# Kernel tuning notes

Measured on AMD Instinct MI355X. Metric: run time of the kernel, lower is better.

## Reference

```python
import jax, jax.numpy as jnp
import numpy as np


def setup_inputs() -> dict:
    key = jax.random.key(0)
    ks = jax.random.split(key, 32)
    def rn(i, shape, s=0.02):
        return jax.random.normal(ks[i], shape, dtype=jnp.float32) * s
    z = lambda n: jnp.zeros((n,), dtype=jnp.float32)
    return {
        'c2': rn(0, (8, 256, 112, 112), 1.0),
        'c3': rn(1, (8, 512, 56, 56), 1.0),
        'c4': rn(2, (8, 1024, 28, 28), 1.0),
        'c5': rn(3, (8, 2048, 14, 14), 1.0),
        'lat_w0': rn(4, (256, 256)),  'lat_b0': z(256),
        'lat_w1': rn(5, (512, 256)),  'lat_b1': z(256),
        'lat_w2': rn(6, (1024, 256)), 'lat_b2': z(256),
        'lat_w3': rn(7, (2048, 256)), 'lat_b3': z(256),
        'sp_w1': rn(8, (2048, 512)), 'sp_b1': z(512),
        'sp_w2': rn(9, (512, 4)),    'sp_b2': z(4),
        'qkv_w': rn(10, (256, 768)), 'qkv_b': z(768),
        'proj_w': rn(11, (256, 256)), 'proj_b': z(256),
        'gat_W': rn(12, (4, 256, 256)),
        'gat_a': rn(13, (4, 512)),
        'out_w': rn(14, (1024, 256)), 'out_b': z(256),
        'label_emb': rn(15, (80, 256), 1.0),
        'spec_w1': rn(16, (256, 128)), 'spec_b1': z(128),
        'spec_w2': rn(17, (128, 80)),  'spec_b2': z(80),
        'spat_w1': rn(18, (256, 128)), 'spat_b1': z(128),
        'spat_w2': rn(19, (128, 80)),  'spat_b2': z(80),
        'gate_w': rn(20, (256, 80)), 'gate_b': z(80),
        'unc_w': rn(21, (256, 80)),  'unc_b': z(80),
    }


def _forward(c2, c3, c4, c5,
             lat_w0, lat_b0, lat_w1, lat_b1, lat_w2, lat_b2, lat_w3, lat_b3,
             sp_w1, sp_b1, sp_w2, sp_b2,
             qkv_w, qkv_b, proj_w, proj_b,
             gat_W, gat_a, out_w, out_b, label_emb,
             spec_w1, spec_b1, spec_w2, spec_b2,
             spat_w1, spat_b1, spat_w2, spat_b2,
             gate_w, gate_b, unc_w, unc_b):
    B = c2.shape[0]
    L = label_emb.shape[0]
    C = 256
    # --- DynamicScaleAwareFPN ---
    pooled = c5.mean(axis=(2, 3))                                   # [B,2048]
    sw = jax.nn.softmax(jax.nn.relu(pooled @ sp_w1 + sp_b1) @ sp_w2 + sp_b2, axis=1)  # [B,4]
    H, W = c2.shape[2], c2.shape[3]
    feats = (c2, c3, c4, c5)
    lws = (lat_w0, lat_w1, lat_w2, lat_w3)
    lbs = (lat_b0, lat_b1, lat_b2, lat_b3)
    fused = jnp.zeros((B, C, H, W), dtype=c2.dtype)
    for i in range(4):  # fixed 4 scales
        l = jnp.einsum('bchw,cd->bdhw', feats[i], lws[i]) + lbs[i][None, :, None, None]
        if l.shape[2] != H or l.shape[3] != W:
            l = jax.image.resize(l, (B, C, H, W), method='bilinear')  # align_corners=False
        fused = fused + l * sw[:, i, None, None, None]
    # --- DeformableAttention (N=H*W > max_tokens=196 -> adaptive pool to 14x14) ---
    th = 14
    x = fused.reshape(B, C, th, H // th, th, W // th).mean(axis=(3, 5))  # exact adaptive avg pool
    x = x.reshape(B, C, th * th).transpose(0, 2, 1)                      # [B,196,C]
    N, nh, hd = th * th, 8, C // 8
    qkv = (x @ qkv_w + qkv_b).reshape(B, N, 3, nh, hd).transpose(2, 0, 3, 1, 4)
    q, k, v = qkv[0], qkv[1], qkv[2]                                     # [B,nh,N,hd]
    attn = jax.nn.softmax(jnp.einsum('bhnd,bhmd->bhnm', q, k) * (hd ** -0.5), axis=-1)
    xo = jnp.einsum('bhnm,bhmd->bhnd', attn, v).transpose(0, 2, 1, 3).reshape(B, N, C)
    xo = xo @ proj_w + proj_b
    gctx = xo.mean(axis=1)                                               # [B,C]
    # --- CrossLabelSemanticGraph (4 GAT heads) ---
    lf = label_emb[None] + gctx[:, None, :]                              # [B,L,C]
    def gat(Wm, avec):
        Wx = lf @ Wm                                                     # [B,L,C]
        # a([Wx_i ; Wx_j]) = Wx_i @ a1 + Wx_j @ a2  (avoids O(L^2*2C) tensor)
        s1 = Wx @ avec[:C]                                               # [B,L]
        s2 = Wx @ avec[C:]                                               # [B,L]
        e = jax.nn.leaky_relu(s1[:, :, None] + s2[:, None, :], 0.2)      # [B,L,L]
        att = jax.nn.softmax(e, axis=2)
        return att @ Wx, att
    heads, atts = jax.vmap(gat)(gat_W, gat_a)                            # [4,B,L,C],[4,B,L,L]
    concat = jnp.moveaxis(heads, 0, 2).reshape(B, L, 4 * C)              # head-order concat
    graph = concat @ out_w + out_b                                       # [B,L,C]
    agg = graph.mean(axis=1)                                             # [B,C]
    # --- SpectralSpatialFusion (dropout inactive at eval) ---
    spec = jax.nn.relu(agg @ spec_w1 + spec_b1) @ spec_w2 + spec_b2
    spat = jax.nn.relu(agg @ spat_w1 + spat_b1) @ spat_w2 + spat_b2
    gate = jax.nn.sigmoid(agg @ gate_w + gate_b)
    logits = gate * spec + (1.0 - gate) * spat
    # --- UncertaintyHead ---
    alpha = jax.nn.softplus(agg @ unc_w + unc_b) + 1.0
    unc = L / jnp.sum(alpha, axis=1, keepdims=True)
    return (logits, spec, spat, gate, unc, sw, atts)


def reference(c2, c3, c4, c5,
              lat_w0, lat_b0, lat_w1, lat_b1, lat_w2, lat_b2, lat_w3, lat_b3,
              sp_w1, sp_b1, sp_w2, sp_b2,
              qkv_w, qkv_b, proj_w, proj_b,
              gat_W, gat_a, out_w, out_b, label_emb,
              spec_w1, spec_b1, spec_w2, spec_b2,
              spat_w1, spat_b1, spat_w2, spat_b2,
              gate_w, gate_b, unc_w, unc_b):
    return _forward(c2, c3, c4, c5,
                    lat_w0, lat_b0, lat_w1, lat_b1, lat_w2, lat_b2, lat_w3, lat_b3,
                    sp_w1, sp_b1, sp_w2, sp_b2,
                    qkv_w, qkv_b, proj_w, proj_b,
                    gat_W, gat_a, out_w, out_b, label_emb,
                    spec_w1, spec_b1, spec_w2, spec_b2,
                    spat_w1, spat_b1, spat_w2, spat_b2,
                    gate_w, gate_b, unc_w, unc_b)
```

## Files before the change

### kernel.cpp

```cpp
#include <hip/hip_runtime.h>
#include <math.h>

typedef __attribute__((ext_vector_type(8))) short bshort8;
typedef __attribute__((ext_vector_type(4))) float f32x4;

#define DI __device__ __forceinline__

DI unsigned short f2bf(float x) {
    unsigned int u = __builtin_bit_cast(unsigned int, x);
    u += 0x7fffu + ((u >> 16) & 1u);
    return (unsigned short)(u >> 16);
}

DI bshort8 pack8(const float* v) {
    bshort8 r;
    #pragma unroll
    for (int j = 0; j < 8; j++) r[j] = (short)f2bf(v[j]);
    return r;
}

DI f32x4 mfma16(bshort8 a, bshort8 b, f32x4 c) {
    return __builtin_amdgcn_mfma_f32_16x16x32_bf16(a, b, c, 0, 0, 0);
}

__device__ const float W14[14][3] = {
    {0.875f, 0.125f, 0.f},
    {0.125f, 0.75f, 0.125f}, {0.125f, 0.75f, 0.125f}, {0.125f, 0.75f, 0.125f},
    {0.125f, 0.75f, 0.125f}, {0.125f, 0.75f, 0.125f}, {0.125f, 0.75f, 0.125f},
    {0.125f, 0.75f, 0.125f}, {0.125f, 0.75f, 0.125f}, {0.125f, 0.75f, 0.125f},
    {0.125f, 0.75f, 0.125f}, {0.125f, 0.75f, 0.125f}, {0.125f, 0.75f, 0.125f},
    {0.125f, 0.875f, 0.f}};
__device__ const float W28[14][4] = {
    {0.5f, 0.4375f, 0.0625f, 0.f},
    {0.0625f, 0.4375f, 0.4375f, 0.0625f}, {0.0625f, 0.4375f, 0.4375f, 0.0625f},
    {0.0625f, 0.4375f, 0.4375f, 0.0625f}, {0.0625f, 0.4375f, 0.4375f, 0.0625f},
    {0.0625f, 0.4375f, 0.4375f, 0.0625f}, {0.0625f, 0.4375f, 0.4375f, 0.0625f},
    {0.0625f, 0.4375f, 0.4375f, 0.0625f}, {0.0625f, 0.4375f, 0.4375f, 0.0625f},
    {0.0625f, 0.4375f, 0.4375f, 0.0625f}, {0.0625f, 0.4375f, 0.4375f, 0.0625f},
    {0.0625f, 0.4375f, 0.4375f, 0.0625f}, {0.0625f, 0.4375f, 0.4375f, 0.0625f},
    {0.0625f, 0.4375f, 0.5f, 0.f}};
__device__ const float W56[14][6] = {
    {0.25f, 0.25f, 0.25f, 0.21875f, 0.03125f, 0.f},
    {0.03125f, 0.21875f, 0.25f, 0.25f, 0.21875f, 0.03125f},
    {0.03125f, 0.21875f, 0.25f, 0.25f, 0.21875f, 0.03125f},
    {0.03125f, 0.21875f, 0.25f, 0.25f, 0.21875f, 0.03125f},
    {0.03125f, 0.21875f, 0.25f, 0.25f, 0.21875f, 0.03125f},
    {0.03125f, 0.21875f, 0.25f, 0.25f, 0.21875f, 0.03125f},
    {0.03125f, 0.21875f, 0.25f, 0.25f, 0.21875f, 0.03125f},
    {0.03125f, 0.21875f, 0.25f, 0.25f, 0.21875f, 0.03125f},
    {0.03125f, 0.21875f, 0.25f, 0.25f, 0.21875f, 0.03125f},
    {0.03125f, 0.21875f, 0.25f, 0.25f, 0.21875f, 0.03125f},
    {0.03125f, 0.21875f, 0.25f, 0.25f, 0.21875f, 0.03125f},
    {0.03125f, 0.21875f, 0.25f, 0.25f, 0.21875f, 0.03125f},
    {0.03125f, 0.21875f, 0.25f, 0.25f, 0.21875f, 0.03125f},
    {0.03125f, 0.21875f, 0.25f, 0.25f, 0.25f, 0.f}};

DI void pool_body112(const float* __restrict__ src, unsigned short* __restrict__ dst,
                     unsigned blk, unsigned t)
{
    unsigned id = blk * 256u + t;
    unsigned p = id / 196u;
    unsigned r = id - p * 196u;
    unsigned ti = r / 14u, tj = r - ti * 14u;
    unsigned b = p >> 8, cin = p & 255u;
    const float* plane = src + (size_t)p * 12544;
    const float4* p4 = (const float4*)(plane + (size_t)(ti * 8) * 112 + tj * 8);
    float4 rv[16];
    #pragma unroll
    for (int i = 0; i < 8; i++) { rv[2 * i] = p4[i * 28]; rv[2 * i + 1] = p4[i * 28 + 1]; }
    float acc = 0.f;
    #pragma unroll
    for (int i = 0; i < 16; i++) acc += (rv[i].x + rv[i].y) + (rv[i].z + rv[i].w);
    dst[(size_t)cin * 1568 + b * 196 + r] = f2bf(acc * (1.f / 64.f));
}

__global__ __launch_bounds__(256) void pool_all(
    const float* __restrict__ c2, const float* __restrict__ c3,
    const float* __restrict__ c4, const float* __restrict__ c5,
    unsigned short* __restrict__ pf0, unsigned short* __restrict__ pf1,
    unsigned short* __restrict__ pf2, unsigned short* __restrict__ pf3,
    float* __restrict__ pooled)
{
    __shared__ alignas(16) float ls[3136];
    unsigned bx = blockIdx.x, t = threadIdx.x;

    if (bx < 1568u) {
        pool_body112(c2, pf0, bx, t);
        return;
    }
    if (bx < 5664u) {
        unsigned p = bx - 1568u;
        unsigned b = p >> 9, cin = p & 511u;
        const float* plane = c3 + (size_t)p * 3136;
        float4* l4 = (float4*)ls;
        const float4* s4 = (const float4*)plane;
        for (int i = t; i < 784; i += 256) l4[i] = s4[i];
        __syncthreads();
        if (t < 196) {
            int ti = t / 14, tj = t - ti * 14;
            int hs = 4 * ti - 1; if (hs < 0) hs = 0;
            int ws = 4 * tj - 1; if (ws < 0) ws = 0;
            float acc = 0.f;
            #pragma unroll
            for (int i = 0; i < 6; i++) {
                int hi = hs + i; if (hi > 55) hi = 55;
                const float* row = ls + hi * 56;
                float rs = 0.f;
                #pragma unroll
                for (int j = 0; j < 6; j++) {
                    int wj = ws + j; if (wj > 55) wj = 55;
                    rs += W56[tj][j] * row[wj];
                }
                acc += W56[ti][i] * rs;
            }
            pf1[(size_t)cin * 1568 + b * 196 + t] = f2bf(acc);
        }
        return;
    }
    if (bx < 13856u) {
        unsigned p = bx - 5664u;
        unsigned b = p >> 10, cin = p & 1023u;
        const float* plane = c4 + (size_t)p * 784;
        float4* l4 = (float4*)ls;
        const float4* s4 = (const float4*)plane;
        if (t < 196) l4[t] = s4[t];
        __syncthreads();
        if (t < 196) {
            int ti = t / 14, tj = t - ti * 14;
            int hs = 2 * ti - 1; if (hs < 0) hs = 0;
            int ws = 2 * tj - 1; if (ws < 0) ws = 0;
            float acc = 0.f;
            #pragma unroll
            for (int i = 0; i < 4; i++) {
                int hi = hs + i; if (hi > 27) hi = 27;
                const float* row = ls + hi * 28;
                float rs = 0.f;
                #pragma unroll
                for (int j = 0; j < 4; j++) {
                    int wj = ws + j; if (wj > 27) wj = 27;
                    rs += W28[tj][j] * row[wj];
                }
                acc += W28[ti][i] * rs;
            }
            pf2[(size_t)cin * 1568 + b * 196 + t] = f2bf(acc);
        }
        return;
    }
    {
        unsigned g = bx - 13856u;
        int wid = t >> 6, lane = t & 63;
        unsigned p = g * 4 + wid;
        unsigned b = p >> 11, cin = p & 2047u;
        const float* plane = c5 + (size_t)p * 196;
        float a0 = plane[lane];
        float a1 = plane[64 + lane];
        float a2 = plane[128 + lane];
        float a3 = (lane < 4) ? plane[192 + lane] : 0.f;
        float* lw = ls + wid * 200;
        lw[lane] = a0; lw[64 + lane] = a1; lw[128 + lane] = a2;
        if (lane < 4) lw[192 + lane] = a3;
        float v = a0 + a1 + a2 + a3;
        #pragma unroll
        for (int off = 32; off > 0; off >>= 1) v += __shfl_xor(v, off, 64);
        if (lane == 0) pooled[p] = v * (1.f / 196.f);
        __syncthreads();
        unsigned short* dst = pf3 + (size_t)cin * 1568 + b * 196;
        #pragma unroll
        for (int rr = 0; rr < 4; rr++) {
            int r = rr * 64 + lane;
            if (r < 196) {
                int ti = r / 14, tj = r - ti * 14;
                int hs = ti - 1; if (hs < 0) hs = 0;
                int ws = tj - 1; if (ws < 0) ws = 0;
                float acc = 0.f;
                #pragma unroll
                for (int i = 0; i < 3; i++) {
                    int hi = hs + i; if (hi > 13) hi = 13;
                    const float* row = lw + hi * 14;
                    float rs = 0.f;
                    #pragma unroll
                    for (int j = 0; j < 3; j++) {
                        int wj = ws + j; if (wj > 13) wj = 13;
                        rs += W14[tj][j] * row[wj];
                    }
                    acc += W14[ti][i] * rs;
                }
                dst[r] = f2bf(acc);
            }
        }
    }
}

__global__ __launch_bounds__(512) void sw_part(
    const float* __restrict__ pooled, const float* __restrict__ sp_w1,
    float* __restrict__ partial,
    const float* __restrict__ gat_W, const float* __restrict__ gat_a,
    float* __restrict__ Wa)
{
    int t = threadIdx.x;
    if (blockIdx.y >= 8) {
        int e = (blockIdx.y - 8) * 8 + blockIdx.x;
        int h = e >> 2, q = e & 3;
        __shared__ float a1[256], a2[256];
        if (t < 256) { a1[t] = gat_a[h * 512 + t]; a2[t] = gat_a[h * 512 + 256 + t]; }
        __syncthreads();
        int w = t >> 6, lane = t & 63;
        #pragma unroll
        for (int ci = 0; ci < 8; ci++) {
            int c = q * 64 + w * 8 + ci;
            const float* row = gat_W + (size_t)h * 65536 + (size_t)c * 256;
            float p1 = 0.f, p2 = 0.f;
            #pragma unroll
            for (int jj = 0; jj < 4; jj++) {
                float v = row[lane + 64 * jj];
                p1 += v * a1[lane + 64 * jj];
                p2 += v * a2[lane + 64 * jj];
            }
            #pragma unroll
            for (int off = 32; off > 0; off >>= 1) {
                p1 += __shfl_xor(p1, off, 64);
                p2 += __shfl_xor(p2, off, 64);
            }
            if (lane == 0) { Wa[h * 512 + c] = p1; Wa[h * 512 + 256 + c] = p2; }
        }
        return;
    }
    int b = blockIdx.x, kc = blockIdx.y;
    __shared__ float ps[256];
    if (t < 256) ps[t] = pooled[b * 2048 + kc * 256 + t];
    __syncthreads();
    float acc = 0.f;
    const float* w = sp_w1 + (size_t)(kc * 256) * 512 + t;
    #pragma unroll 8
    for (int c = 0; c < 256; c++) acc += ps[c] * w[(size_t)c * 512];
    partial[((size_t)b * 8 + kc) * 512 + t] = acc;
}

__global__ __launch_bounds__(512) void sw_fin(
    const float* __restrict__ partial, const float* __restrict__ sp_b1,
    const float* __restrict__ sp_w2, const float* __restrict__ sp_b2,
    const float* __restrict__ lb0, const float* __restrict__ lb1,
    const float* __restrict__ lb2, const float* __restrict__ lb3,
    const float* __restrict__ lemb, const float* __restrict__ Wa,
    float* __restrict__ sw_out, float* __restrict__ xtok,
    float* __restrict__ ldot)
{
    int b = blockIdx.x, t = threadIdx.x;
    __shared__ float h[512];
    __shared__ float s4s[4];
    __shared__ float swl[4];
    __shared__ float bf_s[256];
    float a = sp_b1[t];
    #pragma unroll
    for (int kc = 0; kc < 8; kc++) a += partial[((size_t)b * 8 + kc) * 512 + t];
    h[t] = fmaxf(a, 0.f);
    __syncthreads();
    int wv = t >> 6, lane = t & 63;
    if (wv < 4) {
        float acc = 0.f;
        #pragma unroll
        for (int i = 0; i < 8; i++) {
            int idx = lane + 64 * i;
            acc += h[idx] * sp_w2[idx * 4 + wv];
        }
        #pragma unroll
        for (int off = 32; off > 0; off >>= 1) acc += __shfl_xor(acc, off, 64);
        if (lane == 0) s4s[wv] = acc + sp_b2[wv];
    }
    __syncthreads();
    if (t == 0) {
        float mx = fmaxf(fmaxf(s4s[0], s4s[1]), fmaxf(s4s[2], s4s[3]));
        float e0 = expf(s4s[0] - mx), e1 = expf(s4s[1] - mx);
        float e2 = expf(s4s[2] - mx), e3 = expf(s4s[3] - mx);
        float inv = 1.f / (e0 + e1 + e2 + e3);
        swl[0] = e0 * inv; swl[1] = e1 * inv; swl[2] = e2 * inv; swl[3] = e3 * inv;
        for (int o = 0; o < 4; o++) sw_out[b * 4 + o] = swl[o];
    }
    __syncthreads();
    if (t < 256)
        bf_s[t] = swl[0] * lb0[t] + swl[1] * lb1[t] + swl[2] * lb2[t] + swl[3] * lb3[t];
    {
        int pair = t >> 6;
        #pragma unroll
        for (int r = 0; r < 10; r++) {
            int l = b * 10 + r;
            const float* le = lemb + l * 256 + lane * 4;
            const float* wa = Wa + pair * 256 + lane * 4;
            float p = le[0] * wa[0] + le[1] * wa[1] + le[2] * wa[2] + le[3] * wa[3];
            #pragma unroll
            for (int off = 32; off > 0; off >>= 1) p += __shfl_xor(p, off, 64);
            if (lane == 0) ldot[l * 8 + pair] = p;
        }
    }
    __syncthreads();
    int c = t & 255, half = t >> 8;
    float bv = bf_s[c];
    float* xb = xtok + (size_t)b * 196 * 256 + c;
    for (int r = half; r < 196; r += 2) xb[(size_t)r * 256] = bv;
}

__global__ __launch_bounds__(256) void lateral_slice(
    const unsigned short* __restrict__ pf0, const unsigned short* __restrict__ pf1,
    const unsigned short* __restrict__ pf2, const unsigned short* __restrict__ pf3,
    const float* __restrict__ w0, const float* __restrict__ w1,
    const float* __restrict__ w2, const float* __restrict__ w3,
    const float* __restrict__ sw, float* __restrict__ xtok)
{
    const int sArr[8]    = {0, 1, 2, 2, 3, 3, 3, 3};
    const int koffArr[8] = {0, 0, 0, 512, 0, 512, 1024, 1536};
    const int klenArr[8] = {256, 512, 512, 512, 512, 512, 512, 512};
    int sl = blockIdx.y;
    int s = sArr[sl], koff = koffArr[sl], klen = klenArr[sl];
    const unsigned short* pf = (s == 0) ? pf0 : (s == 1) ? pf1 : (s == 2) ? pf2 : pf3;
    const float* W  = (s == 0) ? w0  : (s == 1) ? w1  : (s == 2) ? w2  : w3;

    int mt = blockIdx.x % 49, nt = blockIdx.x / 49;
    int m0 = mt * 32, n0 = nt * 64;
    __shared__ alignas(16) unsigned short As[1024];
    __shared__ alignas(16) unsigned short Bs[2048];
    int t = threadIdx.x, lane = t & 63, wid = t >> 6;
    int wm = wid >> 1, wn = wid & 1;
    f32x4 acc0 = {0, 0, 0, 0}, acc1 = {0, 0, 0, 0};

    int f = t & 63;
    int mA = m0 + ((t >> 6) & 1) * 16 + (f & 15);
    int kbA = (f >> 4) * 8;
    int nB = n0 + (t >> 6) * 16 + (f & 15);
    int kbB = (f >> 4) * 8;

    unsigned short ark[8];
    float br[8];
    auto loadA = [&](int k0) {
        if (t < 128) {
            const unsigned short* base = pf + (size_t)(koff + k0 + kbA) * 1568 + mA;
            #pragma unroll
            for (int j = 0; j < 8; j++) ark[j] = base[(size_t)j * 1568];
        }
    };
    auto loadB = [&](int k0) {
        const float* base = W + (size_t)(koff + k0 + kbB) * 256 + nB;
        #pragma unroll
        for (int j = 0; j < 8; j++) br[j] = base[(size_t)j * 256];
    };

    loadA(0); loadB(0);
    for (int k0 = 0; k0 < klen; k0 += 32) {
        if (t < 128) {
            bshort8 v8;
            #pragma unroll
            for (int j = 0; j < 8; j++) v8[j] = (short)ark[j];
            *(bshort8*)&As[(((t >> 6) & 1) * 512 + f * 8)] = v8;
        }
        *(bshort8*)&Bs[((t >> 6) * 512 + f * 8)] = pack8(br);
        __syncthreads();
        if (k0 + 32 < klen) { loadA(k0 + 32); loadB(k0 + 32); }
        bshort8 av = *(const bshort8*)&As[wm * 512 + lane * 8];
        bshort8 bv0 = *(const bshort8*)&Bs[(wn * 2 + 0) * 512 + lane * 8];
        bshort8 bv1 = *(const bshort8*)&Bs[(wn * 2 + 1) * 512 + lane * 8];
        acc0 = mfma16(av, bv0, acc0);
        acc1 = mfma16(av, bv1, acc1);
        __syncthreads();
    }
    int col0 = n0 + wn * 32 + (lane & 15);
    int rbase = m0 + wm * 16 + ((lane >> 4) << 2);
    #pragma unroll
    for (int r = 0; r < 4; r++) {
        int m = rbase + r;
        float swv = sw[(m / 196) * 4 + s];
        atomicAdd(&xtok[(size_t)m * 256 + col0], acc0[r] * swv);
        atomicAdd(&xtok[(size_t)m * 256 + col0 + 16], acc1[r] * swv);
    }
}

template <bool B_IS_KXN>
__global__ __launch_bounds__(256) void gemm_kernel(
    const float* __restrict__ Ab, int lda, long long sAy, long long sAz,
    const float* __restrict__ Bb, int ldb, long long sBy, long long sBz,
    float* __restrict__ Cb, int ldc, long long sCy, long long sCz,
    const float* __restrict__ bias, int M, int N, int K,
    float alpha, int mtiles)
{
    const float* A = Ab + blockIdx.y * sAy + blockIdx.z * sAz;
    const float* B = Bb + blockIdx.y * sBy + blockIdx.z * sBz;
    float* C = Cb + blockIdx.y * sCy + blockIdx.z * sCz;
    int mt = blockIdx.x % mtiles, nt = blockIdx.x / mtiles;
    int m0 = mt * 32, n0 = nt * 64;
    __shared__ alignas(16) unsigned short As[1024];
    __shared__ alignas(16) unsigned short Bs[2048];
    int t = threadIdx.x, lane = t & 63, wid = t >> 6;
    int wm = wid >> 1, wn = wid & 1;
    f32x4 acc0 = {0, 0, 0, 0}, acc1 = {0, 0, 0, 0};

    int f = t & 63;
    int mA = m0 + ((t >> 6) & 1) * 16 + (f & 15);
    int kbA = (f >> 4) * 8;
    int nB = n0 + (t >> 6) * 16 + (f & 15);
    int kbB = (f >> 4) * 8;

    float ar[8], br[8];
    auto loadA = [&](int k0) {
        if (t < 128) {
            int kb = k0 + kbA;
            if (mA < M && kb + 8 <= K) {
                const float4* p = (const float4*)(A + (size_t)mA * lda + kb);
                float4 u = p[0], v = p[1];
                ar[0] = u.x; ar[1] = u.y; ar[2] = u.z; ar[3] = u.w;
                ar[4] = v.x; ar[5] = v.y; ar[6] = v.z; ar[7] = v.w;
            } else {
                #pragma unroll
                for (int j = 0; j < 8; j++) {
                    int k = kb + j;
                    ar[j] = (mA < M && k < K) ? A[(size_t)mA * lda + k] : 0.f;
                }
            }
        }
    };
    auto loadB = [&](int k0) {
        int kb = k0 + kbB;
        if constexpr (B_IS_KXN) {
            #pragma unroll
            for (int j = 0; j < 8; j++) {
                int k = kb + j;
                br[j] = (k < K && nB < N) ? B[(size_t)k * ldb + nB] : 0.f;
            }
        } else {
            if (nB < N && kb + 8 <= K) {
                const float4* p = (const float4*)(B + (size_t)nB * ldb + kb);
                float4 u = p[0], v = p[1];
                br[0] = u.x; br[1] = u.y; br[2] = u.z; br[3] = u.w;
                br[4] = v.x; br[5] = v.y; br[6] = v.z; br[7] = v.w;
            } else {
                #pragma unroll
                for (int j = 0; j < 8; j++) {
                    int k = kb + j;
                    br[j] = (nB < N && k < K) ? B[(size_t)nB * ldb + k] : 0.f;
                }
            }
        }
    };

    loadA(0); loadB(0);
    for (int k0 = 0; k0 < K; k0 += 32) {
        if (t < 128) *(bshort8*)&As[(((t >> 6) & 1) * 512 + f * 8)] = pack8(ar);
        *(bshort8*)&Bs[((t >> 6) * 512 + f * 8)] = pack8(br);
        __syncthreads();
        if (k0 + 32 < K) { loadA(k0 + 32); loadB(k0 + 32); }
        bshort8 av = *(const bshort8*)&As[wm * 512 + lane * 8];
        bshort8 bv0 = *(const bshort8*)&Bs[(wn * 2 + 0) * 512 + lane * 8];
        bshort8 bv1 = *(const bshort8*)&Bs[(wn * 2 + 1) * 512 + lane * 8];
        acc0 = mfma16(av, bv0, acc0);
        acc1 = mfma16(av, bv1, acc1);
        __syncthreads();
    }
    int col0 = n0 + wn * 32 + (lane & 15);
    int rbase = m0 + wm * 16 + ((lane >> 4) << 2);
    #pragma unroll
    for (int r = 0; r < 4; r++) {
        int m = rbase + r;
        if (m < M) {
            if (col0 < N) {
                float v = acc0[r] * alpha;
                if (bias) v += bias[col0];
                C[(size_t)m * ldc + col0] = v;
            }
            int c1 = col0 + 16;
            if (c1 < N) {
                float v = acc1[r] * alpha;
                if (bias) v += bias[c1];
                C[(size_t)m * ldc + c1] = v;
            }
        }
    }
}

__global__ __launch_bounds__(256) void fused_attn(
    const float* __restrict__ qkv, float* __restrict__ xo)
{
    int mt = blockIdx.x, h = blockIdx.y, b = blockIdx.z;
    const float* Qb = qkv + (size_t)b * 150528 + h * 32;
    const float* Kb = Qb + 256;
    const float* Vb = Qb + 512;

    __shared__ alignas(16) unsigned short As[1024];
    __shared__ alignas(16) unsigned short Bs[2048];
    __shared__ float Ss[32 * 256];

    int t = threadIdx.x, lane = t & 63, wid = t >> 6;
    int wm = wid >> 1, wn = wid & 1;
    int f = t & 63;
    int m0 = mt * 32;

    if (t < 128) {
        float ar[8];
        int mA = m0 + ((t >> 6) & 1) * 16 + (f & 15);
        int kb = (f >> 4) * 8;
        if (mA < 196) {
            const float4* p = (const float4*)(Qb + (size_t)mA * 768 + kb);
            float4 u = p[0], v = p[1];
            ar[0] = u.x; ar[1] = u.y; ar[2] = u.z; ar[3] = u.w;
            ar[4] = v.x; ar[5] = v.y; ar[6] = v.z; ar[7] = v.w;
        } else {
            #pragma unroll
            for (int j = 0; j < 8; j++) ar[j] = 0.f;
        }
        *(bshort8*)&As[(((t >> 6) & 1) * 512 + f * 8)] = pack8(ar);
    }

    {
        int nBl = (t >> 6) * 16 + (f & 15);
        int kbB = (f >> 4) * 8;
        float br[8];
        auto loadB = [&](int g) {
            int key = g * 64 + nBl;
            if (key < 196) {
                const float4* p = (const float4*)(Kb + (size_t)key * 768 + kbB);
                float4 u = p[0], v = p[1];
                br[0] = u.x; br[1] = u.y; br[2] = u.z; br[3] = u.w;
                br[4] = v.x; br[5] = v.y; br[6] = v.z; br[7] = v.w;
            } else {
                #pragma unroll
                for (int j = 0; j < 8; j++) br[j] = 0.f;
            }
        };
        loadB(0);
        for (int g = 0; g < 4; g++) {
            __syncthreads();
            *(bshort8*)&Bs[((t >> 6) * 512 + f * 8)] = pack8(br);
            __syncthreads();
            if (g < 3) loadB(g + 1);
            f32x4 acc0 = {0, 0, 0, 0}, acc1 = {0, 0, 0, 0};
            bshort8 av = *(const bshort8*)&As[wm * 512 + lane * 8];
            bshort8 bv0 = *(const bshort8*)&Bs[(wn * 2 + 0) * 512 + lane * 8];
            bshort8 bv1 = *(const bshort8*)&Bs[(wn * 2 + 1) * 512 + lane * 8];
            acc0 = mfma16(av, bv0, acc0);
            acc1 = mfma16(av, bv1, acc1);
            int col0 = g * 64 + wn * 32 + (lane & 15);
            int rbase = wm * 16 + ((lane >> 4) << 2);
            #pragma unroll
            for (int r = 0; r < 4; r++) {
                Ss[(rbase + r) * 256 + col0]      = acc0[r] * 0.17677669529663687f;
                Ss[(rbase + r) * 256 + col0 + 16] = acc1[r] * 0.17677669529663687f;
            }
        }
    }
    __syncthreads();

    {
        #pragma unroll
        for (int i = 0; i < 8; i++) {
            float* p = Ss + (wid * 8 + i) * 256;
            float v0 = p[lane], v1 = p[64 + lane], v2 = p[128 + lane];
            float v3 = (lane < 4) ? p[192 + lane] : -1e30f;
            float mx = fmaxf(fmaxf(v0, v1), fmaxf(v2, v3));
            #pragma unroll
            for (int off = 32; off > 0; off >>= 1) mx = fmaxf(mx, __shfl_xor(mx, off, 64));
            float e0 = expf(v0 - mx), e1 = expf(v1 - mx), e2 = expf(v2 - mx);
            float e3 = (lane < 4) ? expf(v3 - mx) : 0.f;
            float sum = e0 + e1 + e2 + e3;
            #pragma unroll
            for (int off = 32; off > 0; off >>= 1) sum += __shfl_xor(sum, off, 64);
            float inv = 1.f / sum;
            p[lane] = e0 * inv;
            p[64 + lane] = e1 * inv;
            p[128 + lane] = e2 * inv;
            if (lane < 4) p[192 + lane] = e3 * inv;
            else          p[192 + lane] = 0.f;
        }
    }
    __syncthreads();

    {
        f32x4 acc0 = {0, 0, 0, 0}, acc1 = {0, 0, 0, 0};
        int nBl = (t >> 6) * 16 + (f & 15);
        int kbB = (f >> 4) * 8;
        int mAl = ((t >> 6) & 1) * 16 + (f & 15);
        int kbA = (f >> 4) * 8;
        float ar[8], br[8];
        auto loadA = [&](int k0) {
            if (t < 128) {
                #pragma unroll
                for (int j = 0; j < 8; j++) ar[j] = Ss[mAl * 256 + k0 + kbA + j];
            }
        };
        auto loadB = [&](int k0) {
            #pragma unroll
            for (int j = 0; j < 8; j++) {
                int k = k0 + kbB + j;
                br[j] = (k < 196 && nBl < 32) ? Vb[(size_t)k * 768 + nBl] : 0.f;
            }
        };
        loadA(0); loadB(0);
        for (int k0 = 0; k0 < 256; k0 += 32) {
            __syncthreads();
            if (t < 128) *(bshort8*)&As[(((t >> 6) & 1) * 512 + f * 8)] = pack8(ar);
            *(bshort8*)&Bs[((t >> 6) * 512 + f * 8)] = pack8(br);
            __syncthreads();
            if (k0 + 32 < 256) { loadA(k0 + 32); loadB(k0 + 32); }
            bshort8 av = *(const bshort8*)&As[wm * 512 + lane * 8];
            bshort8 bv0 = *(const bshort8*)&Bs[(wn * 2 + 0) * 512 + lane * 8];
            bshort8 bv1 = *(const bshort8*)&Bs[(wn * 2 + 1) * 512 + lane * 8];
            acc0 = mfma16(av, bv0, acc0);
            acc1 = mfma16(av, bv1, acc1);
        }
        int col0 = wn * 32 + (lane & 15);
        int rbase = wm * 16 + ((lane >> 4) << 2);
        if (col0 < 32) {
            #pragma unroll
            for (int r = 0; r < 4; r++) {
                int m = m0 + rbase + r;
                if (m < 196) {
                    xo[((size_t)b * 196 + m) * 256 + h * 32 + col0]      = acc0[r];
                    xo[((size_t)b * 196 + m) * 256 + h * 32 + col0 + 16] = acc1[r];
                }
            }
        }
    }
}

__global__ __launch_bounds__(1024) void tail1(
    const float* __restrict__ xo, const float* __restrict__ proj_w,
    const float* __restrict__ proj_b,
    const float* __restrict__ gat_W, const float* __restrict__ lemb,
    const float* __restrict__ Wa, const float* __restrict__ ldot,
    float* __restrict__ atts, float* __restrict__ hm_g)
{
    int b = blockIdx.x >> 2, h = blockIdx.x & 3;
    int t = threadIdx.x, lane = t & 63, wv = t >> 6;
    __shared__ float red[1024];
    __shared__ float xm[256];
    __shared__ float gctx_s[256];
    __shared__ float gdot_s[2];
    __shared__ float s12h[160];
    __shared__ float am_s[80];
    __shared__ float av_s[256];

    {
        int c = t & 255, sl = t >> 8;
        const float* base = xo + ((size_t)b * 196 + sl * 49) * 256 + c;
        float s = 0.f;
        #pragma unroll 7
        for (int i = 0; i < 49; i++) s += base[(size_t)i * 256];
        red[t] = s;
    }
    if (t < 80) am_s[t] = 0.f;
    __syncthreads();
    if (t < 256) xm[t] = (red[t] + red[256 + t] + red[512 + t] + red[768 + t]) * (1.f / 196.f);
    __syncthreads();

    {
        int n = t & 255, ks = t >> 8;
        float acc = 0.f;
        const float* w = proj_w + (size_t)(ks * 64) * 256 + n;
        #pragma unroll 8
        for (int i = 0; i < 64; i++) acc += xm[ks * 64 + i] * w[(size_t)i * 256];
        red[t] = acc;
    }
    __syncthreads();
    if (t < 256) gctx_s[t] = proj_b[t] + red[t] + red[256 + t] + red[512 + t] + red[768 + t];
    __syncthreads();

    if (wv < 2) {
        int pair = h * 2 + wv;
        const float* wa = Wa + pair * 256 + lane * 4;
        float p = gctx_s[lane * 4] * wa[0] + gctx_s[lane * 4 + 1] * wa[1]
                + gctx_s[lane * 4 + 2] * wa[2] + gctx_s[lane * 4 + 3] * wa[3];
        #pragma unroll
        for (int off = 32; off > 0; off >>= 1) p += __shfl_xor(p, off, 64);
        if (lane == 0) gdot_s[wv] = p;
    }
    __syncthreads();
    if (t < 160) {
        int q = t / 80, l = t - q * 80;
        s12h[t] = ldot[l * 8 + h * 2 + q] + gdot_s[q];
    }
    __syncthreads();

    {
        #pragma unroll
        for (int rr = 0; rr < 5; rr++) {
            int i = rr * 16 + wv;
            float s1i = s12h[i];
            const float* s2 = s12h + 80;
            float v0 = s1i + s2[lane]; v0 = v0 > 0.f ? v0 : 0.2f * v0;
            float v1 = -1e30f;
            if (lane < 16) { v1 = s1i + s2[64 + lane]; v1 = v1 > 0.f ? v1 : 0.2f * v1; }
            float mx = fmaxf(v0, v1);
            #pragma unroll
            for (int off = 32; off > 0; off >>= 1) mx = fmaxf(mx, __shfl_xor(mx, off, 64));
            float e0 = expf(v0 - mx), e1 = (lane < 16) ? expf(v1 - mx) : 0.f;
            float sum = e0 + e1;
            #pragma unroll
            for (int off = 32; off > 0; off >>= 1) sum += __shfl_xor(sum, off, 64);
            float inv = 1.f / sum;
            float* orow = atts + (size_t)h * 51200 + b * 6400 + i * 80;
            float p0 = e0 * inv;
            orow[lane] = p0;
            atomicAdd(&am_s[lane], p0);
            if (lane < 16) {
                float p1 = e1 * inv;
                orow[64 + lane] = p1;
                atomicAdd(&am_s[64 + lane], p1);
            }
        }
    }
    __syncthreads();

    {
        int n = t & 255, ks = t >> 8;
        float acc = 0.f;
        const float* le = lemb + n;
        #pragma unroll 5
        for (int l = ks * 20; l < ks * 20 + 20; l++) acc += am_s[l] * le[(size_t)l * 256];
        red[t] = acc;
    }
    __syncthreads();
    if (t < 256)
        av_s[t] = (red[t] + red[256 + t] + red[512 + t] + red[768 + t]) * (1.f / 80.f)
                + gctx_s[t];
    __syncthreads();
    {
        int n = t & 255, ks = t >> 8;
        float acc = 0.f;
        const float* w = gat_W + (size_t)h * 65536 + (size_t)(ks * 64) * 256 + n;
        #pragma unroll 8
        for (int i = 0; i < 64; i++) acc += av_s[ks * 64 + i] * w[(size_t)i * 256];
        red[t] = acc;
    }
    __syncthreads();
    if (t < 256)
        hm_g[(b * 4 + h) * 256 + t] = red[t] + red[256 + t] + red[512 + t] + red[768 + t];
}

__global__ __launch_bounds__(1024) void tail2(
    const float* __restrict__ hm_g,
    const float* __restrict__ out_w, const float* __restrict__ out_b,
    const float* __restrict__ spec_w1, const float* __restrict__ spec_b1,
    const float* __restrict__ spec_w2, const float* __restrict__ spec_b2,
    const float* __restrict__ spat_w1, const float* __restrict__ spat_b1,
    const float* __restrict__ spat_w2, const float* __restrict__ spat_b2,
    const float* __restrict__ gate_w, const float* __restrict__ gate_b,
    const float* __restrict__ unc_w, const float* __restrict__ unc_b,
    float* __restrict__ out)
{
    int b = blockIdx.x, t = threadIdx.x;
    __shared__ float red[1024];
    __shared__ float as_s[256];
    __shared__ float hb_s[256];
    __shared__ float fv_s[320];

    {
        int n = t & 255, ks = t >> 8;
        float acc = 0.f;
        const float* hv = hm_g + b * 1024 + ks * 256;
        const float* w = out_w + (size_t)(ks * 256) * 256 + n;
        #pragma unroll 8
        for (int k = 0; k < 256; k++) acc += hv[k] * w[(size_t)k * 256];
        red[t] = acc;
    }
    __syncthreads();
    if (t < 256) as_s[t] = out_b[t] + red[t] + red[256 + t] + red[512 + t] + red[768 + t];
    __syncthreads();

    {
        int u = t & 255, ks = t >> 8;
        int which = u >> 7, oo = u & 127;
        const float* w1 = which ? spat_w1 : spec_w1;
        float acc = 0.f;
        #pragma unroll 8
        for (int i = 0; i < 64; i++) {
            int k = ks * 64 + i;
            acc += as_s[k] * w1[(size_t)k * 128 + oo];
        }
        red[t] = acc;
    }
    __syncthreads();
    if (t < 256) {
        int which = t >> 7, oo = t & 127;
        const float* b1 = which ? spat_b1 : spec_b1;
        hb_s[t] = fmaxf(red[t] + red[256 + t] + red[512 + t] + red[768 + t] + b1[oo], 0.f);
    }
    __syncthreads();

    if (t < 960) {
        int sub = t / 320, u = t - sub * 320;
        int head = u / 80, o = u - head * 80;
        const float* wp; const float* src; int K;
        if (head == 0)      { wp = spec_w2; src = hb_s;       K = 128; }
        else if (head == 1) { wp = spat_w2; src = hb_s + 128; K = 128; }
        else if (head == 2) { wp = gate_w;  src = as_s;       K = 256; }
        else                { wp = unc_w;   src = as_s;       K = 256; }
        int k0 = (K * sub) / 3, k1 = (K * (sub + 1)) / 3;
        float acc = 0.f;
        for (int k = k0; k < k1; k++) acc += src[k] * wp[(size_t)k * 80 + o];
        red[sub * 320 + u] = acc;
    }
    __syncthreads();
    if (t < 320) {
        int head = t / 80, o = t - head * 80;
        const float* bp = head == 0 ? spec_b2 : head == 1 ? spat_b2 : head == 2 ? gate_b : unc_b;
        fv_s[t] = red[t] + red[320 + t] + red[640 + t] + bp[o];
    }
    __syncthreads();

    if (t < 80) {
        float sp = fv_s[t], st2 = fv_s[80 + t], gz = fv_s[160 + t], uz = fv_s[240 + t];
        float g = 1.f / (1.f + expf(-gz));
        out[b * 80 + t] = g * sp + (1.f - g) * st2;
        out[640 + b * 80 + t] = sp;
        out[1280 + b * 80 + t] = st2;
        out[1920 + b * 80 + t] = g;
        red[t] = log1pf(expf(uz)) + 1.f;
    }
    __syncthreads();
    if (t == 0) {
        float s = 0.f;
        for (int l = 0; l < 80; l++) s += red[l];
        out[2560 + b] = 80.f / s;
    }
}

extern "C" void kernel_launch(void* const* d_in, const int* in_sizes, int n_in,
                              void* d_out, int out_size, void* d_ws, size_t ws_size,
                              hipStream_t stream)
{
    (void)in_sizes; (void)n_in; (void)out_size; (void)ws_size;
    const float* c2 = (const float*)d_in[0];
    const float* c3 = (const float*)d_in[1];
    const float* c4 = (const float*)d_in[2];
    const float* c5 = (const float*)d_in[3];
    const float* lat_w0 = (const float*)d_in[4];
    const float* lat_b0 = (const float*)d_in[5];
    const float* lat_w1 = (const float*)d_in[6];
    const float* lat_b1 = (const float*)d_in[7];
    const float* lat_w2 = (const float*)d_in[8];
    const float* lat_b2 = (const float*)d_in[9];
    const float* lat_w3 = (const float*)d_in[10];
    const float* lat_b3 = (const float*)d_in[11];
    const float* sp_w1 = (const float*)d_in[12];
    const float* sp_b1 = (const float*)d_in[13];
    const float* sp_w2 = (const float*)d_in[14];
    const float* sp_b2 = (const float*)d_in[15];
    const float* qkv_w = (const float*)d_in[16];
    const float* qkv_b = (const float*)d_in[17];
    const float* proj_w = (const float*)d_in[18];
    const float* proj_b = (const float*)d_in[19];
    const float* gat_W = (const float*)d_in[20];
    const float* gat_a = (const float*)d_in[21];
    const float* out_w = (const float*)d_in[22];
    const float* out_b = (const float*)d_in[23];
    const float* label_emb = (const float*)d_in[24];
    const float* spec_w1 = (const float*)d_in[25];
    const float* spec_b1 = (const float*)d_in[26];
    const float* spec_w2 = (const float*)d_in[27];
    const float* spec_b2 = (const float*)d_in[28];
    const float* spat_w1 = (const float*)d_in[29];
    const float* spat_b1 = (const float*)d_in[30];
    const float* spat_w2 = (const float*)d_in[31];
    const float* spat_b2 = (const float*)d_in[32];
    const float* gate_w = (const float*)d_in[33];
    const float* gate_b = (const float*)d_in[34];
    const float* unc_w = (const float*)d_in[35];
    const float* unc_b = (const float*)d_in[36];

    float* out = (float*)d_out;
    float* ws = (float*)d_ws;

    unsigned short* pf0 = (unsigned short*)(ws + 0);
    unsigned short* pf1 = (unsigned short*)(ws + 401408);
    unsigned short* pf2 = (unsigned short*)(ws + 1204224);
    unsigned short* pf3 = (unsigned short*)(ws + 2809856);
    float* pooled = ws + 6021120;
    float* swpart = ws + 6039552;
    float* Wa     = ws + 6072320;
    float* ldot   = ws + 6074368;
    float* qkv    = ws + 0;
    float* xo     = ws + 3662848;
    float* hm_g   = ws + 4253696;
    float* xtok   = ws + 6106112;

    float* swp  = out + 2568;
    float* atts = out + 2600;

    pool_all<<<17952, 256, 0, stream>>>(c2, c3, c4, c5, pf0, pf1, pf2, pf3, pooled);
    sw_part<<<dim3(8, 10), 512, 0, stream>>>(pooled, sp_w1, swpart, gat_W, gat_a, Wa);
    sw_fin<<<8, 512, 0, stream>>>(swpart, sp_b1, sp_w2, sp_b2,
                                  lat_b0, lat_b1, lat_b2, lat_b3,
                                  label_emb, Wa, swp, xtok, ldot);
    lateral_slice<<<dim3(196, 8), 256, 0, stream>>>(pf0, pf1, pf2, pf3,
                                                    lat_w0, lat_w1, lat_w2, lat_w3,
                                                    swp, xtok);
    gemm_kernel<true><<<dim3(49 * 12, 1, 1), 256, 0, stream>>>(
        xtok, 256, 0, 0, qkv_w, 768, 0, 0, qkv, 768, 0, 0,
        qkv_b, 1568, 768, 256, 1.f, 49);
    fused_attn<<<dim3(7, 8, 8), 256, 0, stream>>>(qkv, xo);
    tail1<<<32, 1024, 0, stream>>>(xo, proj_w, proj_b, gat_W, label_emb,
                                   Wa, ldot, atts, hm_g);
    tail2<<<8, 1024, 0, stream>>>(hm_g, out_w, out_b,
                                  spec_w1, spec_b1, spec_w2, spec_b2,
                                  spat_w1, spat_b1, spat_w2, spat_b2,
                                  gate_w, gate_b, unc_w, unc_b, out);
}
```

Baseline: 460.7 us.

## Batch pooling planes per block, move GAT Wa into pool kernel, fuse token-mean via atomics

The c4 and c5 pooling paths now handle 4 and 16 planes per block, which cuts the block count roughly in half. The c5 shared-memory rows are padded to a stride of 15 to reduce bank conflicts. The gat_W·a projection moves from sw_part into extra pool_all blocks. The per-batch token mean is now accumulated with atomicAdd in fused_attn's epilogue instead of re-reading xo in tail1, with sw_fin zeroing the accumulator beforehand. This trades atomic contention and float summation-order nondeterminism for fewer blocks and less memory traffic.

```diff
diff --git a/kernel.cpp b/kernel.cpp
--- a/kernel.cpp
+++ b/kernel.cpp
@@ -79,9 +79,11 @@
     const float* __restrict__ c4, const float* __restrict__ c5,
     unsigned short* __restrict__ pf0, unsigned short* __restrict__ pf1,
     unsigned short* __restrict__ pf2, unsigned short* __restrict__ pf3,
-    float* __restrict__ pooled)
+    float* __restrict__ pooled,
+    const float* __restrict__ gat_W, const float* __restrict__ gat_a,
+    float* __restrict__ Wa)
 {
-    __shared__ alignas(16) float ls[3136];
+    __shared__ alignas(16) float ls[3360];
     unsigned bx = blockIdx.x, t = threadIdx.x;
 
     if (bx < 1568u) {
@@ -117,23 +119,24 @@
         }
         return;
     }
-    if (bx < 13856u) {
-        unsigned p = bx - 5664u;
-        unsigned b = p >> 10, cin = p & 1023u;
-        const float* plane = c4 + (size_t)p * 784;
+    if (bx < 7712u) {
+        unsigned g = bx - 5664u;
+        unsigned p0 = g * 4;
         float4* l4 = (float4*)ls;
-        const float4* s4 = (const float4*)plane;
-        if (t < 196) l4[t] = s4[t];
+        const float4* s4 = (const float4*)(c4 + (size_t)p0 * 784);
+        for (int i = t; i < 784; i += 256) l4[i] = s4[i];
         __syncthreads();
-        if (t < 196) {
-            int ti = t / 14, tj = t - ti * 14;
+        for (int o = t; o < 784; o += 256) {
+            int pl = o / 196, r = o - pl * 196;
+            int ti = r / 14, tj = r - ti * 14;
             int hs = 2 * ti - 1; if (hs < 0) hs = 0;
             int ws = 2 * tj - 1; if (ws < 0) ws = 0;
+            const float* base = ls + pl * 784;
             float acc = 0.f;
             #pragma unroll
             for (int i = 0; i < 4; i++) {
                 int hi = hs + i; if (hi > 27) hi = 27;
-                const float* row = ls + hi * 28;
+                const float* row = base + hi * 28;
                 float rs = 0.f;
                 #pragma unroll
                 for (int j = 0; j < 4; j++) {
@@ -142,72 +145,88 @@
                 }
                 acc += W28[ti][i] * rs;
             }
-            pf2[(size_t)cin * 1568 + b * 196 + t] = f2bf(acc);
+            unsigned p = p0 + pl;
+            unsigned b = p >> 10, cin = p & 1023u;
+            pf2[(size_t)cin * 1568 + b * 196 + r] = f2bf(acc);
         }
         return;
     }
-    {
-        unsigned g = bx - 13856u;
+    if (bx < 8736u) {
+        unsigned g = bx - 7712u;
         int wid = t >> 6, lane = t & 63;
-        unsigned p = g * 4 + wid;
-        unsigned b = p >> 11, cin = p & 2047u;
-        const float* plane = c5 + (size_t)p * 196;
-        float a0 = plane[lane];
-        float a1 = plane[64 + lane];
-        float a2 = plane[128 + lane];
-        float a3 = (lane < 4) ? plane[192 + lane] : 0.f;
-        float* lw = ls + wid * 200;
-        lw[lane] = a0; lw[64 + lane] = a1; lw[128 + lane] = a2;
-        if (lane < 4) lw[192 + lane] = a3;
-        float v = a0 + a1 + a2 + a3;
+        unsigned pbase = g * 16 + wid * 4;
+        float* lw = ls + wid * 840;
         #pragma unroll
-        for (int off = 32; off > 0; off >>= 1) v += __shfl_xor(v, off, 64);
-        if (lane == 0) pooled[p] = v * (1.f / 196.f);
+        for (int sub = 0; sub < 4; sub++) {
+            unsigned p = pbase + sub;
+            const float* plane = c5 + (size_t)p * 196;
+            float a0 = plane[lane];
+            float a1 = plane[64 + lane];
+            float a2 = plane[128 + lane];
+            float a3 = (lane < 4) ? plane[192 + lane] : 0.f;
+            float* lp = lw + sub * 210;
+            {
+                int i0 = lane,        r0 = i0 / 14, c0 = i0 - r0 * 14;
+                int i1 = 64 + lane,   r1 = i1 / 14, c1 = i1 - r1 * 14;
+                int i2 = 128 + lane,  r2 = i2 / 14, c2 = i2 - r2 * 14;
+                lp[r0 * 15 + c0] = a0;
+                lp[r1 * 15 + c1] = a1;
+                lp[r2 * 15 + c2] = a2;
+                if (lane < 4) {
+                    int i3 = 192 + lane, r3 = i3 / 14, c3 = i3 - r3 * 14;
+                    lp[r3 * 15 + c3] = a3;
+                }
+            }
+            float v = a0 + a1 + a2 + a3;
+            #pragma unroll
+            for (int off = 32; off > 0; off >>= 1) v += __shfl_xor(v, off, 64);
+            if (lane == 0) pooled[p] = v * (1.f / 196.f);
+        }
         __syncthreads();
-        unsigned short* dst = pf3 + (size_t)cin * 1568 + b * 196;
         #pragma unroll
-        for (int rr = 0; rr < 4; rr++) {
-            int r = rr * 64 + lane;
-            if (r < 196) {
-                int ti = r / 14, tj = r - ti * 14;
-                int hs = ti - 1; if (hs < 0) hs = 0;
-                int ws = tj - 1; if (ws < 0) ws = 0;
-                float acc = 0.f;
-                #pragma unroll
-                for (int i = 0; i < 3; i++) {
-                    int hi = hs + i; if (hi > 13) hi = 13;
-                    const float* row = lw + hi * 14;
-                    float rs = 0.f;
+        for (int sub = 0; sub < 4; sub++) {
+            unsigned p = pbase + sub;
+            unsigned b = p >> 11, cin = p & 2047u;
+            const float* lp = lw + sub * 210;
+            unsigned short* dst = pf3 + (size_t)cin * 1568 + b * 196;
+            #pragma unroll
+            for (int rr = 0; rr < 4; rr++) {
+                int r = rr * 64 + lane;
+                if (r < 196) {
+                    int ti = r / 14, tj = r - ti * 14;
+                    int hs = ti - 1; if (hs < 0) hs = 0;
+                    int ws = tj - 1; if (ws < 0) ws = 0;
+                    float acc = 0.f;
                     #pragma unroll
-                    for (int j = 0; j < 3; j++) {
-                        int wj = ws + j; if (wj > 13) wj = 13;
-                        rs += W14[tj][j] * row[wj];
+                    for (int i = 0; i < 3; i++) {
+                        int hi = hs + i; if (hi > 13) hi = 13;
+                        const float* row = lp + hi * 15;
+                        float rs = 0.f;
+                        #pragma unroll
+                        for (int j = 0; j < 3; j++) {
+                            int wj = ws + j; if (wj > 13) wj = 13;
+                            rs += W14[tj][j] * row[wj];
+                        }
+                        acc += W14[ti][i] * rs;
                     }
-                    acc += W14[ti][i] * rs;
+                    dst[r] = f2bf(acc);
                 }
-                dst[r] = f2bf(acc);
-            }
-        }
-    }
-}
-
-__global__ __launch_bounds__(512) void sw_part(
-    const float* __restrict__ pooled, const float* __restrict__ sp_w1,
-    float* __restrict__ partial,
-    const float* __restrict__ gat_W, const float* __restrict__ gat_a,
-    float* __restrict__ Wa)
-{
-    int t = threadIdx.x;
-    if (blockIdx.y >= 8) {
-        int e = (blockIdx.y - 8) * 8 + blockIdx.x;
+            }
+        }
+        return;
+    }
+    {
+        unsigned e = bx - 8736u;
         int h = e >> 2, q = e & 3;
-        __shared__ float a1[256], a2[256];
-        if (t < 256) { a1[t] = gat_a[h * 512 + t]; a2[t] = gat_a[h * 512 + 256 + t]; }
+        float* a1 = ls;
+        float* a2 = ls + 256;
+        a1[t] = gat_a[h * 512 + t];
+        a2[t] = gat_a[h * 512 + 256 + t];
         __syncthreads();
         int w = t >> 6, lane = t & 63;
         #pragma unroll
-        for (int ci = 0; ci < 8; ci++) {
-            int c = q * 64 + w * 8 + ci;
+        for (int ci = 0; ci < 16; ci++) {
+            int c = q * 64 + w * 16 + ci;
             const float* row = gat_W + (size_t)h * 65536 + (size_t)c * 256;
             float p1 = 0.f, p2 = 0.f;
             #pragma unroll
@@ -223,8 +242,14 @@
             }
             if (lane == 0) { Wa[h * 512 + c] = p1; Wa[h * 512 + 256 + c] = p2; }
         }
-        return;
-    }
+    }
+}
+
+__global__ __launch_bounds__(512) void sw_part(
+    const float* __restrict__ pooled, const float* __restrict__ sp_w1,
+    float* __restrict__ partial)
+{
+    int t = threadIdx.x;
     int b = blockIdx.x, kc = blockIdx.y;
     __shared__ float ps[256];
     if (t < 256) ps[t] = pooled[b * 2048 + kc * 256 + t];
@@ -243,13 +268,14 @@
     const float* __restrict__ lb2, const float* __restrict__ lb3,
     const float* __restrict__ lemb, const float* __restrict__ Wa,
     float* __restrict__ sw_out, float* __restrict__ xtok,
-    float* __restrict__ ldot)
+    float* __restrict__ ldot, float* __restrict__ xmsum)
 {
     int b = blockIdx.x, t = threadIdx.x;
     __shared__ float h[512];
     __shared__ float s4s[4];
     __shared__ float swl[4];
     __shared__ float bf_s[256];
+    if (t < 256) xmsum[b * 256 + t] = 0.f;
     float a = sp_b1[t];
     #pragma unroll
     for (int kc = 0; kc < 8; kc++) a += partial[((size_t)b * 8 + kc) * 512 + t];
@@ -474,7 +500,8 @@
 }
 
 __global__ __launch_bounds__(256) void fused_attn(
-    const float* __restrict__ qkv, float* __restrict__ xo)
+    const float* __restrict__ qkv, float* __restrict__ xo,
+    float* __restrict__ xmsum)
 {
     int mt = blockIdx.x, h = blockIdx.y, b = blockIdx.z;
     const float* Qb = qkv + (size_t)b * 150528 + h * 32;
@@ -605,20 +632,25 @@
         int col0 = wn * 32 + (lane & 15);
         int rbase = wm * 16 + ((lane >> 4) << 2);
         if (col0 < 32) {
+            float s0 = 0.f, s1 = 0.f;
             #pragma unroll
             for (int r = 0; r < 4; r++) {
                 int m = m0 + rbase + r;
                 if (m < 196) {
                     xo[((size_t)b * 196 + m) * 256 + h * 32 + col0]      = acc0[r];
                     xo[((size_t)b * 196 + m) * 256 + h * 32 + col0 + 16] = acc1[r];
+                    s0 += acc0[r];
+                    s1 += acc1[r];
                 }
             }
+            atomicAdd(&xmsum[b * 256 + h * 32 + col0], s0);
+            atomicAdd(&xmsum[b * 256 + h * 32 + col0 + 16], s1);
         }
     }
 }
 
 __global__ __launch_bounds__(1024) void tail1(
-    const float* __restrict__ xo, const float* __restrict__ proj_w,
+    const float* __restrict__ xmsum, const float* __restrict__ proj_w,
     const float* __restrict__ proj_b,
     const float* __restrict__ gat_W, const float* __restrict__ lemb,
     const float* __restrict__ Wa, const float* __restrict__ ldot,
@@ -634,17 +666,8 @@
     __shared__ float am_s[80];
     __shared__ float av_s[256];
 
-    {
-        int c = t & 255, sl = t >> 8;
-        const float* base = xo + ((size_t)b * 196 + sl * 49) * 256 + c;
-        float s = 0.f;
-        #pragma unroll 7
-        for (int i = 0; i < 49; i++) s += base[(size_t)i * 256];
-        red[t] = s;
-    }
+    if (t < 256) xm[t] = xmsum[b * 256 + t] * (1.f / 196.f);
     if (t < 80) am_s[t] = 0.f;
-    __syncthreads();
-    if (t < 256) xm[t] = (red[t] + red[256 + t] + red[512 + t] + red[768 + t]) * (1.f / 196.f);
     __syncthreads();
 
     {
@@ -873,6 +896,7 @@
     float* swpart = ws + 6039552;
     float* Wa     = ws + 6072320;
     float* ldot   = ws + 6074368;
+    float* xmsum  = ws + 6075008;
     float* qkv    = ws + 0;
     float* xo     = ws + 3662848;
     float* hm_g   = ws + 4253696;
@@ -881,19 +905,20 @@
     float* swp  = out + 2568;
     float* atts = out + 2600;
 
-    pool_all<<<17952, 256, 0, stream>>>(c2, c3, c4, c5, pf0, pf1, pf2, pf3, pooled);
-    sw_part<<<dim3(8, 10), 512, 0, stream>>>(pooled, sp_w1, swpart, gat_W, gat_a, Wa);
+    pool_all<<<8752, 256, 0, stream>>>(c2, c3, c4, c5, pf0, pf1, pf2, pf3, pooled,
+                                       gat_W, gat_a, Wa);
+    sw_part<<<dim3(8, 8), 512, 0, stream>>>(pooled, sp_w1, swpart);
     sw_fin<<<8, 512, 0, stream>>>(swpart, sp_b1, sp_w2, sp_b2,
                                   lat_b0, lat_b1, lat_b2, lat_b3,
-                                  label_emb, Wa, swp, xtok, ldot);
+                                  label_emb, Wa, swp, xtok, ldot, xmsum);
     lateral_slice<<<dim3(196, 8), 256, 0, stream>>>(pf0, pf1, pf2, pf3,
                                                     lat_w0, lat_w1, lat_w2, lat_w3,
                                                     swp, xtok);
     gemm_kernel<true><<<dim3(49 * 12, 1, 1), 256, 0, stream>>>(
         xtok, 256, 0, 0, qkv_w, 768, 0, 0, qkv, 768, 0, 0,
         qkv_b, 1568, 768, 256, 1.f, 49);
-    fused_attn<<<dim3(7, 8, 8), 256, 0, stream>>>(qkv, xo);
-    tail1<<<32, 1024, 0, stream>>>(xo, proj_w, proj_b, gat_W, label_emb,
+    fused_attn<<<dim3(7, 8, 8), 256, 0, stream>>>(qkv, xo, xmsum);
+    tail1<<<32, 1024, 0, stream>>>(xmsum, proj_w, proj_b, gat_W, label_emb,
                                    Wa, ldot, atts, hm_g);
     tail2<<<8, 1024, 0, stream>>>(hm_g, out_w, out_b,
                                   spec_w1, spec_b1, spec_w2, spec_b2,
```

Result: slower. 473.8 us (+2.8%).
